# Kernel optimization log

Hardware: AMD Instinct MI355X
Metric: run time of the kernel (lower is better)

The kernel has to match this reference:

```python
import jax, jax.numpy as jnp
import numpy as np

NUM_GROUPS = 8
EPS = 1e-5


def setup_inputs() -> dict:
    key = jax.random.key(0)
    ks = jax.random.split(key, 10)
    b, c, h, w = 4, 64, 64, 64
    x = jax.random.normal(ks[0], (b, c, h, w), dtype=jnp.float32)
    # GroupNorm affine params (default init: weight=1, bias=0; randomize slightly for testing)
    gamma = jnp.ones((c,), jnp.float32) + 0.01 * jax.random.normal(ks[1], (c,))
    beta = 0.01 * jax.random.normal(ks[2], (c,))
    # 1x1 conv weights as [out_c, in_c] matrices (xavier-uniform), biases zeros in torch init
    def xavier(k, shape):
        fan = shape[0] + shape[1]
        lim = jnp.sqrt(6.0 / fan)
        return jax.random.uniform(k, shape, jnp.float32, -lim, lim)
    Wq = xavier(ks[3], (c, c)); bq = jnp.zeros((c,), jnp.float32)
    Wk = xavier(ks[4], (c, c)); bk = jnp.zeros((c,), jnp.float32)
    Wv = xavier(ks[5], (c, c)); bv = jnp.zeros((c,), jnp.float32)
    Wp = xavier(ks[6], (c, c)); bp = jnp.zeros((c,), jnp.float32)
    return {"x": x, "gamma": gamma, "beta": beta,
            "Wq": Wq, "bq": bq, "Wk": Wk, "bk": bk,
            "Wv": Wv, "bv": bv, "Wp": Wp, "bp": bp}


def group_norm(x, gamma, beta):
    b, c, h, w = x.shape
    g = NUM_GROUPS
    xg = x.reshape(b, g, c // g, h, w)
    mean = jnp.mean(xg, axis=(2, 3, 4), keepdims=True)
    var = jnp.var(xg, axis=(2, 3, 4), keepdims=True)
    xn = ((xg - mean) * jax.lax.rsqrt(var + EPS)).reshape(b, c, h, w)
    return xn * gamma[None, :, None, None] + beta[None, :, None, None]


def reference(x, gamma, beta, Wq, bq, Wk, bk, Wv, bv, Wp, bp):
    b, c, h, w = x.shape
    n = h * w
    xn = group_norm(x, gamma, beta)
    xn_flat = xn.reshape(b, c, n)  # [b, c, n]
    # 1x1 convs == channel-wise linear maps
    q = jnp.einsum('oc,bcn->bno', Wq, xn_flat) + bq  # [b, n, c]
    k = jnp.einsum('oc,bcn->bon', Wk, xn_flat) + bk[None, :, None]  # [b, c, n]
    v = jnp.einsum('oc,bcn->bno', Wv, xn_flat) + bv  # [b, n, c]
    attn = jax.nn.softmax(jnp.einsum('bnc,bcm->bnm', q, k) / jnp.sqrt(jnp.float32(c)), axis=-1)
    out = jnp.einsum('bnm,bmc->bnc', attn, v)  # [b, n, c]
    out = out.transpose(0, 2, 1).reshape(b, c, h, w)
    out = jnp.einsum('oc,bchw->bohw', Wp, out) + bp[None, :, None, None]
    return out + x
```

## Files before the change

### kernel.cpp

```cpp
#include <hip/hip_runtime.h>
#include <hip/hip_bf16.h>
#include <math.h>

#define BATCH 4
#define CH    64
#define NPOS  4096
#define NGRP  8
#define CPG   8
#define GEPS  1e-5f
#define NSPLIT 8
#define LOG2E 1.4426950408889634f

typedef __attribute__((ext_vector_type(8))) short bf16x8;
typedef __attribute__((ext_vector_type(4))) float f32x4;

__device__ __forceinline__ ushort f2bf(float f) {
    union { float f; uint32_t u; } v; v.f = f;
    uint32_t r = v.u + 0x7fffu + ((v.u >> 16) & 1u);
    return (ushort)(r >> 16);
}
__device__ __forceinline__ float bf2f(ushort u) {
    union { uint32_t u; float f; } v; v.u = ((uint32_t)u) << 16; return v.f;
}

__device__ __forceinline__ uint32_t swz(uint32_t row, uint32_t byteInRow) {
    return (row << 7) + (byteInRow ^ ((row & 7u) << 4));
}

__device__ __forceinline__ bf16x8 ldfrag(const ushort* base, int row, int kbyte) {
    return *(const bf16x8*)((const char*)base + swz(row, kbyte));
}

__global__ __launch_bounds__(256) void gn_part_kernel(const float* __restrict__ x,
                                                      float2* __restrict__ part) {
    const int blk = blockIdx.x;
    const float4* xp4 = (const float4*)(x + (size_t)blk * 4096);
    float s1 = 0.f, s2 = 0.f;
    for (int i = threadIdx.x; i < 1024; i += 256) {
        float4 t = xp4[i];
        s1 += t.x + t.y + t.z + t.w;
        s2 += t.x * t.x + t.y * t.y + t.z * t.z + t.w * t.w;
    }
    __shared__ float sh1[256], sh2[256];
    const int tid = threadIdx.x;
    sh1[tid] = s1; sh2[tid] = s2;
    __syncthreads();
    for (int off = 128; off > 0; off >>= 1) {
        if (tid < off) { sh1[tid] += sh1[tid + off]; sh2[tid] += sh2[tid + off]; }
        __syncthreads();
    }
    if (tid == 0) { float2 r; r.x = sh1[0]; r.y = sh2[0]; part[blk] = r; }
}

__global__ __launch_bounds__(256) void qkv_mfma_kernel(
    const float* __restrict__ x, const float2* __restrict__ part,
    const float* __restrict__ gamma, const float* __restrict__ beta,
    const float* __restrict__ Wq, const float* __restrict__ bq,
    const float* __restrict__ Wk, const float* __restrict__ bk,
    const float* __restrict__ Wv, const float* __restrict__ bv,
    ushort* __restrict__ qg, ushort* __restrict__ kg, ushort* __restrict__ vg)
{
    __shared__ ushort xn[64 * 64];
    __shared__ ushort Wl[64 * 64];
    __shared__ ushort ob[64 * 64];
    __shared__ float st[16];

    const int tid = threadIdx.x;
    const int w = tid >> 6, lane = tid & 63, g = lane >> 4, q16 = lane & 15;
    const int m = blockIdx.x >> 8;
    const int bidx = blockIdx.x & 255;
    const int b = bidx >> 6, n0 = (bidx & 63) << 6;

    const float* W = (m == 0) ? Wq : (m == 1) ? Wk : Wv;

    {
        const int row = tid >> 2, cb = (tid & 3) << 4;
#pragma unroll
        for (int j = 0; j < 4; ++j) {
            float4 v = *(const float4*)(W + row * 64 + cb + j * 4);
            ushort4 h; h.x = f2bf(v.x); h.y = f2bf(v.y); h.z = f2bf(v.z); h.w = f2bf(v.w);
            *(ushort4*)((char*)Wl + swz(row, (cb + j * 4) * 2)) = h;
        }
    }
    if (tid < 64) {
        float2 p = part[b * 64 + tid];
        float s1 = p.x, s2 = p.y;
        s1 += __shfl_xor(s1, 1); s2 += __shfl_xor(s2, 1);
        s1 += __shfl_xor(s1, 2); s2 += __shfl_xor(s2, 2);
        s1 += __shfl_xor(s1, 4); s2 += __shfl_xor(s2, 4);
        if ((tid & 7) == 0) {
            const float inv = 1.0f / (float)(CPG * NPOS);
            float mean = s1 * inv;
            float var  = s2 * inv - mean * mean;
            st[(tid >> 3) * 2]     = mean;
            st[(tid >> 3) * 2 + 1] = rsqrtf(var + GEPS);
        }
    }
    __syncthreads();

    {
        const int c = tid >> 2, nb = (tid & 3) << 4;
        const float mean = st[(c >> 3) * 2];
        const float rstd = st[(c >> 3) * 2 + 1];
        const float gmm = gamma[c] * rstd;
        const float btt = beta[c] - mean * gmm;
        const float* xp = x + (((size_t)(b * CH + c)) << 12) + n0 + nb;
#pragma unroll
        for (int j = 0; j < 4; ++j) {
            float4 v = *(const float4*)(xp + j * 4);
            float vv[4] = {v.x, v.y, v.z, v.w};
#pragma unroll
            for (int e = 0; e < 4; ++e) {
                int n = nb + j * 4 + e;
                *(ushort*)((char*)xn + swz(n, c * 2)) = f2bf(vv[e] * gmm + btt);
            }
        }
    }
    __syncthreads();

    if (m < 2) {
        const float* bias = m ? bk : bq;
        const float scl = m ? 1.0f : 0.125f * LOG2E;
        bf16x8 ax0 = ldfrag(xn, (w << 4) + q16, (g << 4));
        bf16x8 ax1 = ldfrag(xn, (w << 4) + q16, 64 + (g << 4));
#pragma unroll
        for (int ot = 0; ot < 4; ++ot) {
            f32x4 acc = {0.f, 0.f, 0.f, 0.f};
            bf16x8 b0 = ldfrag(Wl, (ot << 4) + q16, (g << 4));
            bf16x8 b1 = ldfrag(Wl, (ot << 4) + q16, 64 + (g << 4));
            acc = __builtin_amdgcn_mfma_f32_16x16x32_bf16(ax0, b0, acc, 0, 0, 0);
            acc = __builtin_amdgcn_mfma_f32_16x16x32_bf16(ax1, b1, acc, 0, 0, 0);
            float bs = bias[(ot << 4) + q16];
#pragma unroll
            for (int r = 0; r < 4; ++r)
                *(ushort*)((char*)ob + swz((w << 4) + (g << 2) + r, ((ot << 4) + q16) << 1)) =
                    f2bf((acc[r] + bs) * scl);
        }
        __syncthreads();
        ushort* dst = (m ? kg : qg) + (((size_t)b) << 18);
#pragma unroll
        for (int i = 0; i < 2; ++i) {
            const int G = tid + (i << 8);
            const int lane_ = G & 63;
            const int h = (G >> 6) & 1;
            const int colb = (h << 5) + ((lane_ >> 4) << 3);
            if (m == 0) {
                const int qgi = (G >> 7) & 1;
                const int qgl = G >> 8;
                const int row = (qgl << 5) + (qgi << 4) + (lane_ & 15);
                int4 d = *(const int4*)((char*)ob + swz(row, colb << 1));
                *(int4*)(dst + (((size_t)(n0 >> 5) + qgl) << 11)
                             + ((size_t)((((qgi << 1) + h) << 6) + lane_) << 3)) = d;
            } else {
                const int nt = G >> 7;
                const int row = (nt << 4) + (lane_ & 15);
                int4 d = *(const int4*)((char*)ob + swz(row, colb << 1));
                *(int4*)(dst + ((size_t)(n0 >> 6) << 12)
                             + ((size_t)((((nt << 1) + h) << 6) + lane_) << 3)) = d;
            }
        }
    } else {
        bf16x8 aw0 = ldfrag(Wl, (w << 4) + q16, (g << 4));
        bf16x8 aw1 = ldfrag(Wl, (w << 4) + q16, 64 + (g << 4));
#pragma unroll
        for (int nt = 0; nt < 4; ++nt) {
            f32x4 acc = {0.f, 0.f, 0.f, 0.f};
            bf16x8 b0 = ldfrag(xn, (nt << 4) + q16, (g << 4));
            bf16x8 b1 = ldfrag(xn, (nt << 4) + q16, 64 + (g << 4));
            acc = __builtin_amdgcn_mfma_f32_16x16x32_bf16(aw0, b0, acc, 0, 0, 0);
            acc = __builtin_amdgcn_mfma_f32_16x16x32_bf16(aw1, b1, acc, 0, 0, 0);
#pragma unroll
            for (int r = 0; r < 4; ++r) {
                float bs = bv[(w << 4) + (g << 2) + r];
                *(ushort*)((char*)ob + swz((w << 4) + (g << 2) + r, ((nt << 4) + q16) << 1)) =
                    f2bf(acc[r] + bs);
            }
        }
        __syncthreads();
        ushort* dst = vg + (((size_t)b) << 18) + ((size_t)(n0 >> 6) << 12);
#pragma unroll
        for (int i = 0; i < 2; ++i) {
            const int G = tid + (i << 8);
            const int lane_ = G & 63;
            const int h = (G >> 6) & 1;
            const int ct = G >> 7;
            const int row = (ct << 4) + (lane_ & 15);
            const int colb = (h << 5) + ((lane_ >> 4) << 3);
            int4 d = *(const int4*)((char*)ob + swz(row, colb << 1));
            *(int4*)(dst + ((size_t)((((ct << 1) + h) << 6) + lane_) << 3)) = d;
        }
    }
}

#define LOADK(KF, KT)                                                          \
    _Pragma("unroll") for (int nt = 0; nt < 4; ++nt)                           \
    _Pragma("unroll") for (int h = 0; h < 2; ++h)                              \
        KF[nt][h] = *(const bf16x8*)(kp + (((size_t)(KT)) << 12) +             \
                     ((size_t)((((nt << 1) + h) << 6) + lane) << 3));

#define STEP(KF, KFN, KT, PREF)                                                \
  do {                                                                         \
    bf16x8 vf[4][2];                                                           \
    _Pragma("unroll") for (int ct = 0; ct < 4; ++ct)                           \
    _Pragma("unroll") for (int h = 0; h < 2; ++h)                              \
        vf[ct][h] = *(const bf16x8*)(vp + (((size_t)(KT)) << 12) +             \
                     ((size_t)((((ct << 1) + h) << 6) + lane) << 3));          \
    if (PREF) { LOADK(KFN, (KT) + 1); }                                        \
    f32x4 s_[4][2];                                                            \
    _Pragma("unroll") for (int nt = 0; nt < 4; ++nt)                           \
    _Pragma("unroll") for (int qgi = 0; qgi < 2; ++qgi) {                      \
        f32x4 z = {0.f, 0.f, 0.f, 0.f};                                        \
        z = __builtin_amdgcn_mfma_f32_16x16x32_bf16(KF[nt][0], aq[qgi][0], z, 0, 0, 0); \
        z = __builtin_amdgcn_mfma_f32_16x16x32_bf16(KF[nt][1], aq[qgi][1], z, 0, 0, 0); \
        s_[nt][qgi] = z;                                                       \
    }                                                                          \
    _Pragma("unroll") for (int qgi = 0; qgi < 2; ++qgi) {                      \
        _Pragma("unroll") for (int nt = 0; nt < 4; ++nt) {                     \
            float p0 = exp2f(s_[nt][qgi][0]);                                  \
            float p1 = exp2f(s_[nt][qgi][1]);                                  \
            float p2 = exp2f(s_[nt][qgi][2]);                                  \
            float p3 = exp2f(s_[nt][qgi][3]);                                  \
            l_[qgi] += (p0 + p1) + (p2 + p3);                                  \
            float2 t01; t01.x = p0; t01.y = p1;                                \
            float2 t23; t23.x = p2; t23.y = p3;                                \
            __hip_bfloat162 b01 = __float22bfloat162_rn(t01);                  \
            __hip_bfloat162 b23 = __float22bfloat162_rn(t23);                  \
            uint2 pk; pk.x = *(uint32_t*)&b01; pk.y = *(uint32_t*)&b23;        \
            *(uint2*)((char*)Pw + swz((qgi << 4) + q16, (nt << 5) + (lg << 3))) = pk; \
        }                                                                      \
    }                                                                          \
    asm volatile("" ::: "memory");                                             \
    bf16x8 pb[2][2];                                                           \
    _Pragma("unroll") for (int qgi = 0; qgi < 2; ++qgi) {                      \
        pb[qgi][0] = ldfrag(Pw, (qgi << 4) + q16, (lg << 4));                  \
        pb[qgi][1] = ldfrag(Pw, (qgi << 4) + q16, 64 + (lg << 4));             \
    }                                                                          \
    _Pragma("unroll") for (int ct = 0; ct < 4; ++ct)                           \
    _Pragma("unroll") for (int qgi = 0; qgi < 2; ++qgi) {                      \
        f32x4 o = o_[ct][qgi];                                                 \
        o = __builtin_amdgcn_mfma_f32_16x16x32_bf16(vf[ct][0], pb[qgi][0], o, 0, 0, 0); \
        o = __builtin_amdgcn_mfma_f32_16x16x32_bf16(vf[ct][1], pb[qgi][1], o, 0, 0, 0); \
        o_[ct][qgi] = o;                                                       \
    }                                                                          \
  } while (0)

__global__ __launch_bounds__(256) void attn_mfma_kernel(
    const ushort* __restrict__ qg, const ushort* __restrict__ kg,
    const ushort* __restrict__ vg,
    ushort* __restrict__ opart, float* __restrict__ lpart)
{
    __shared__ ushort Ps[4][32 * 64];

    const int tid = threadIdx.x;
    const int w = tid >> 6, lane = tid & 63, lg = lane >> 4, q16 = lane & 15;
    const int logical = ((blockIdx.x & 7) << 7) + (blockIdx.x >> 3);
    const int ks = logical & 7;
    const int qb = (logical >> 3) & 31;
    const int b  = logical >> 8;
    const int q0 = (qb << 7) + (w << 5);
    const ushort* qp = qg + (((size_t)b) << 18) + ((size_t)((qb << 2) + w) << 11);
    const ushort* kp = kg + (((size_t)b) << 18) + ((size_t)ks << 15);
    const ushort* vp = vg + (((size_t)b) << 18) + ((size_t)ks << 15);
    ushort* Pw = Ps[w];

    bf16x8 aq[2][2];
#pragma unroll
    for (int qgi = 0; qgi < 2; ++qgi)
#pragma unroll
        for (int h = 0; h < 2; ++h)
            aq[qgi][h] = *(const bf16x8*)(qp + ((size_t)((((qgi << 1) + h) << 6) + lane) << 3));

    float l_[2] = {0.f, 0.f};
    f32x4 o_[4][2];
#pragma unroll
    for (int ct = 0; ct < 4; ++ct)
#pragma unroll
        for (int qgi = 0; qgi < 2; ++qgi) o_[ct][qgi] = (f32x4){0.f, 0.f, 0.f, 0.f};

    bf16x8 kfA[4][2], kfB[4][2];
    LOADK(kfA, 0);

#pragma unroll 1
    for (int kt2 = 0; kt2 < 8; kt2 += 2) {
        STEP(kfA, kfB, kt2, true);
        STEP(kfB, kfA, kt2 + 1, (kt2 + 1) < 7);
    }

#pragma unroll
    for (int qgi = 0; qgi < 2; ++qgi) {
        l_[qgi] += __shfl_xor(l_[qgi], 16);
        l_[qgi] += __shfl_xor(l_[qgi], 32);
    }

    const size_t bs = (size_t)(b * NSPLIT + ks);
#pragma unroll
    for (int qgi = 0; qgi < 2; ++qgi) {
        const int n = q0 + (qgi << 4) + q16;
        ushort* ob = opart + ((bs * 64) << 12) + n;
#pragma unroll
        for (int ct = 0; ct < 4; ++ct)
#pragma unroll
            for (int r = 0; r < 4; ++r)
                ob[((size_t)((ct << 4) + (lg << 2) + r)) << 12] = f2bf(o_[ct][qgi][r]);
    }
    if (lg == 0) {
#pragma unroll
        for (int qgi = 0; qgi < 2; ++qgi) {
            const int n = q0 + (qgi << 4) + q16;
            lpart[bs * 4096 + n] = l_[qgi];
        }
    }
}

__global__ __launch_bounds__(256) void combine_kernel(
    const ushort* __restrict__ opart, const float* __restrict__ lpart,
    const float* __restrict__ x, const float* __restrict__ Wp,
    const float* __restrict__ bp, float* __restrict__ out)
{
    __shared__ ushort Obf[64 * 64];
    __shared__ ushort Wps[64 * 64];
    __shared__ float as_[64];

    const int tid = threadIdx.x;
    const int w = tid >> 6, lane = tid & 63, g = lane >> 4, q16 = lane & 15;
    const int xcd = blockIdx.x & 7, idx = blockIdx.x >> 3;
    const int b = xcd >> 1;
    const int n0 = ((((xcd & 1) << 5) + idx) << 6);

    {
        const int row = tid >> 2, cb = (tid & 3) << 4;
#pragma unroll
        for (int j = 0; j < 4; ++j) {
            float4 v = *(const float4*)(Wp + row * 64 + cb + j * 4);
            ushort4 h; h.x = f2bf(v.x); h.y = f2bf(v.y); h.z = f2bf(v.z); h.w = f2bf(v.w);
            *(ushort4*)((char*)Wps + swz(row, (cb + j * 4) * 2)) = h;
        }
    }
    if (tid < 64) {
        const int n = n0 + tid;
        float d = 0.f;
#pragma unroll
        for (int s = 0; s < NSPLIT; ++s)
            d += lpart[(size_t)(b * NSPLIT + s) * 4096 + n];
        as_[tid] = 1.0f / d;
    }
    __syncthreads();

    {
        const int c = tid >> 2, nb = (tid & 3) << 4;
        const ushort* base = opart + ((((size_t)(b * NSPLIT)) * 64 + c) << 12) + n0 + nb;
        const size_t sstride = (size_t)64 << 12;
        float acc[16];
#pragma unroll
        for (int e = 0; e < 16; ++e) acc[e] = 0.f;
#pragma unroll
        for (int s = 0; s < NSPLIT; ++s) {
            const ushort* p = base + s * sstride;
            uint4 d0 = *(const uint4*)(p);
            uint4 d1 = *(const uint4*)(p + 8);
            const uint uw[8] = {d0.x, d0.y, d0.z, d0.w, d1.x, d1.y, d1.z, d1.w};
#pragma unroll
            for (int j = 0; j < 8; ++j) {
                acc[2 * j]     += bf2f((ushort)(uw[j] & 0xffffu));
                acc[2 * j + 1] += bf2f((ushort)(uw[j] >> 16));
            }
        }
#pragma unroll
        for (int e = 0; e < 16; ++e) {
            int nl = nb + e;
            *(ushort*)((char*)Obf + swz(nl, c << 1)) = f2bf(acc[e] * as_[nl]);
        }
    }
    __syncthreads();

    {
        bf16x8 aw0 = ldfrag(Wps, (w << 4) + q16, (g << 4));
        bf16x8 aw1 = ldfrag(Wps, (w << 4) + q16, 64 + (g << 4));
        float bpv[4];
#pragma unroll
        for (int r = 0; r < 4; ++r) bpv[r] = bp[(w << 4) + (g << 2) + r];
#pragma unroll
        for (int qt = 0; qt < 4; ++qt) {
            f32x4 d = {0.f, 0.f, 0.f, 0.f};
            bf16x8 b0 = ldfrag(Obf, (qt << 4) + q16, (g << 4));
            bf16x8 b1 = ldfrag(Obf, (qt << 4) + q16, 64 + (g << 4));
            d = __builtin_amdgcn_mfma_f32_16x16x32_bf16(aw0, b0, d, 0, 0, 0);
            d = __builtin_amdgcn_mfma_f32_16x16x32_bf16(aw1, b1, d, 0, 0, 0);
#pragma unroll
            for (int r = 0; r < 4; ++r) {
                int oc = (w << 4) + (g << 2) + r;
                size_t addr = (((size_t)(b * CH + oc)) << 12) + n0 + (qt << 4) + q16;
                out[addr] = d[r] + bpv[r] + x[addr];
            }
        }
    }
}

extern "C" void kernel_launch(void* const* d_in, const int* in_sizes, int n_in,
                              void* d_out, int out_size, void* d_ws, size_t ws_size,
                              hipStream_t stream) {
    const float* x     = (const float*)d_in[0];
    const float* gamma = (const float*)d_in[1];
    const float* beta  = (const float*)d_in[2];
    const float* Wq    = (const float*)d_in[3];
    const float* bq    = (const float*)d_in[4];
    const float* Wk    = (const float*)d_in[5];
    const float* bk    = (const float*)d_in[6];
    const float* Wv    = (const float*)d_in[7];
    const float* bv    = (const float*)d_in[8];
    const float* Wp    = (const float*)d_in[9];
    const float* bp    = (const float*)d_in[10];
    float* out = (float*)d_out;

    float2* part = (float2*)d_ws;
    ushort* q_t = (ushort*)((char*)d_ws + 4096);
    ushort* k_t = q_t + (size_t)BATCH * NPOS * CH;
    ushort* v_t = k_t + (size_t)BATCH * NPOS * CH;
    ushort* opart = (ushort*)((char*)d_ws + 4096 + (size_t)3 * BATCH * NPOS * CH * 2);
    float* lpart = (float*)((char*)opart + (size_t)BATCH * NSPLIT * CH * NPOS * 2);

    hipLaunchKernelGGL(gn_part_kernel, dim3(256), dim3(256), 0, stream, x, part);
    hipLaunchKernelGGL(qkv_mfma_kernel, dim3(768), dim3(256), 0, stream,
                       x, part, gamma, beta, Wq, bq, Wk, bk, Wv, bv, q_t, k_t, v_t);
    hipLaunchKernelGGL(attn_mfma_kernel, dim3(1024), dim3(256), 0, stream,
                       q_t, k_t, v_t, opart, lpart);
    hipLaunchKernelGGL(combine_kernel, dim3(BATCH * 64), dim3(256), 0, stream,
                       opart, lpart, x, Wp, bp, out);
}
```

Measured before the change: 51.43 us.

## Store attention partial outputs in fragment-native layout for coalesced writes

The attention kernel now writes its partial output accumulators in the MFMA fragment order, one contiguous 8-byte ushort4 per lane, instead of scattered 2-byte stores strided by 4096 elements across channels. The combine kernel reads this new layout with matching per-lane uint2 loads and writes the reduced result into shared memory as ushort4 chunks. The aim is to remove uncoalesced global stores in the attention epilogue, at the cost of coupling the partial buffer layout tightly to both kernels' thread mappings.

```diff
diff --git a/kernel.cpp b/kernel.cpp
--- a/kernel.cpp
+++ b/kernel.cpp
@@ -293,16 +293,19 @@
     }
 
     const size_t bs = (size_t)(b * NSPLIT + ks);
-#pragma unroll
-    for (int qgi = 0; qgi < 2; ++qgi) {
-        const int n = q0 + (qgi << 4) + q16;
-        ushort* ob = opart + ((bs * 64) << 12) + n;
-#pragma unroll
-        for (int ct = 0; ct < 4; ++ct)
-#pragma unroll
-            for (int r = 0; r < 4; ++r)
-                ob[((size_t)((ct << 4) + (lg << 2) + r)) << 12] = f2bf(o_[ct][qgi][r]);
-    }
+    const int qw = (qb << 2) + w;
+    ushort* ob = opart + (((bs << 7) + qw) << 11);
+#pragma unroll
+    for (int ct = 0; ct < 4; ++ct)
+#pragma unroll
+        for (int qgi = 0; qgi < 2; ++qgi) {
+            ushort4 h;
+            h.x = f2bf(o_[ct][qgi][0]);
+            h.y = f2bf(o_[ct][qgi][1]);
+            h.z = f2bf(o_[ct][qgi][2]);
+            h.w = f2bf(o_[ct][qgi][3]);
+            *(ushort4*)(ob + (((((ct << 1) + qgi) << 6) + lane) << 2)) = h;
+        }
     if (lg == 0) {
 #pragma unroll
         for (int qgi = 0; qgi < 2; ++qgi) {
@@ -322,7 +325,8 @@
     __shared__ float as_[64];
 
     const int tid = threadIdx.x;
-    const int w = tid >> 6, lane = tid & 63, g = lane >> 4, q16 = lane & 15;
+    const int w = tid >> 6, lane = tid & 63, lg = lane >> 4, q16 = lane & 15;
+    const int g = lg;
     const int xcd = blockIdx.x & 7, idx = blockIdx.x >> 3;
     const int b = xcd >> 1;
     const int n0 = ((((xcd & 1) << 5) + idx) << 6);
@@ -347,29 +351,43 @@
     __syncthreads();
 
     {
-        const int c = tid >> 2, nb = (tid & 3) << 4;
-        const ushort* base = opart + ((((size_t)(b * NSPLIT)) * 64 + c) << 12) + n0 + nb;
-        const size_t sstride = (size_t)64 << 12;
-        float acc[16];
-#pragma unroll
-        for (int e = 0; e < 16; ++e) acc[e] = 0.f;
+        const int qw0 = n0 >> 5;
+        float acc[2][2][4];
+#pragma unroll
+        for (int qwi = 0; qwi < 2; ++qwi)
+#pragma unroll
+            for (int qgi = 0; qgi < 2; ++qgi)
+#pragma unroll
+                for (int r = 0; r < 4; ++r) acc[qwi][qgi][r] = 0.f;
 #pragma unroll
         for (int s = 0; s < NSPLIT; ++s) {
-            const ushort* p = base + s * sstride;
-            uint4 d0 = *(const uint4*)(p);
-            uint4 d1 = *(const uint4*)(p + 8);
-            const uint uw[8] = {d0.x, d0.y, d0.z, d0.w, d1.x, d1.y, d1.z, d1.w};
-#pragma unroll
-            for (int j = 0; j < 8; ++j) {
-                acc[2 * j]     += bf2f((ushort)(uw[j] & 0xffffu));
-                acc[2 * j + 1] += bf2f((ushort)(uw[j] >> 16));
+            const size_t bs = (size_t)(b * NSPLIT + s);
+#pragma unroll
+            for (int qwi = 0; qwi < 2; ++qwi)
+#pragma unroll
+                for (int qgi = 0; qgi < 2; ++qgi) {
+                    uint2 d = *(const uint2*)(opart + (((bs << 7) + qw0 + qwi) << 11)
+                                              + (((((w << 1) + qgi) << 6) + lane) << 2));
+                    acc[qwi][qgi][0] += bf2f((ushort)(d.x & 0xffffu));
+                    acc[qwi][qgi][1] += bf2f((ushort)(d.x >> 16));
+                    acc[qwi][qgi][2] += bf2f((ushort)(d.y & 0xffffu));
+                    acc[qwi][qgi][3] += bf2f((ushort)(d.y >> 16));
+                }
+        }
+        const int c0b = ((w << 4) + (lg << 2)) << 1;
+#pragma unroll
+        for (int qwi = 0; qwi < 2; ++qwi)
+#pragma unroll
+            for (int qgi = 0; qgi < 2; ++qgi) {
+                const int nl = (qwi << 5) + (qgi << 4) + q16;
+                const float a = as_[nl];
+                ushort4 h;
+                h.x = f2bf(acc[qwi][qgi][0] * a);
+                h.y = f2bf(acc[qwi][qgi][1] * a);
+                h.z = f2bf(acc[qwi][qgi][2] * a);
+                h.w = f2bf(acc[qwi][qgi][3] * a);
+                *(ushort4*)((char*)Obf + swz(nl, c0b)) = h;
             }
-        }
-#pragma unroll
-        for (int e = 0; e < 16; ++e) {
-            int nl = nb + e;
-            *(ushort*)((char*)Obf + swz(nl, c << 1)) = f2bf(acc[e] * as_[nl]);
-        }
     }
     __syncthreads();
 
```

Result: no change. 50.70 us (median of 2 runs) (-1.4%).
